# Optimization experiments

Measured on AMD Instinct MI355X. Metric: run time of the kernel, lower is better.

Reference implementation:

```python
import jax, jax.numpy as jnp
import numpy as np

N, E, D = 100000, 640000, 128  # nodes, edges, feature dim (in_dim == out_dim == 128)
BN_EPS = 1e-5


def setup_inputs() -> dict:
    key = jax.random.key(0)
    ks = jax.random.split(key, 8)
    x = jax.random.normal(ks[0], (N, D), dtype=jnp.float32)
    edge_index = jax.random.randint(ks[1], (2, E), 0, N, dtype=jnp.int64)
    s = 1.0 / np.sqrt(D)
    W1 = jax.random.uniform(ks[2], (D, D), jnp.float32, -s, s)
    b1 = jax.random.uniform(ks[3], (D,), jnp.float32, -s, s)
    W2 = jax.random.uniform(ks[4], (D, D), jnp.float32, -s, s)
    b2 = jax.random.uniform(ks[5], (D,), jnp.float32, -s, s)
    return {
        "x": x,
        "edge_index": edge_index,
        "eps": jnp.array([0.1], dtype=jnp.float32),
        "W1": W1, "b1": b1,
        "g1": jnp.ones((D,), jnp.float32), "beta1": jnp.zeros((D,), jnp.float32),
        "W2": W2, "b2": b2,
        "g2": jnp.ones((D,), jnp.float32), "beta2": jnp.zeros((D,), jnp.float32),
    }


def _batchnorm(h, gamma, beta):
    # BatchNorm1d in training mode: biased batch stats over the node dim
    mean = jnp.mean(h, axis=0)
    var = jnp.var(h, axis=0)
    return gamma * (h - mean) * jax.lax.rsqrt(var + BN_EPS) + beta


def reference(x, edge_index, eps, W1, b1, g1, beta1, W2, b2, g2, beta2):
    src, dst = edge_index[0], edge_index[1]
    # gather messages from source nodes, scatter-add into destination nodes
    aggr = jax.ops.segment_sum(x[src], dst, num_segments=x.shape[0])  # [N, D]
    h = (1.0 + eps) * x + aggr
    h = jax.nn.relu(_batchnorm(h @ W1.T + b1, g1, beta1))
    h = jax.nn.relu(_batchnorm(h @ W2.T + b2, g2, beta2))
    return h
```

## Files before the change

### kernel.cpp

```cpp
#include <hip/hip_runtime.h>

#define NN 100000
#define DD 128
#define EE 640000
#define NPAD 100352
#define NCHUNK 391

typedef __bf16 bf16x8 __attribute__((ext_vector_type(8)));
typedef float floatx4 __attribute__((ext_vector_type(4)));

union FragU { int4 i; bf16x8 b; unsigned short us[8]; };

__device__ __forceinline__ unsigned short f2bf(float f) {
    unsigned int u = __float_as_uint(f);
    u += 0x7FFF + ((u >> 16) & 1);
    return (unsigned short)(u >> 16);
}

#define HBLK 2500
#define XBLK 3200
__global__ __launch_bounds__(256) void pre_k(
    const int* __restrict__ ei, int* __restrict__ deg,
    const float4* __restrict__ x4, ushort4* __restrict__ xb4,
    const float4* __restrict__ W1, const float4* __restrict__ W2,
    ushort4* __restrict__ wb1, ushort4* __restrict__ wb2) {
    int bid = blockIdx.x;
    if (bid < HBLK) {
        int e = bid * 256 + threadIdx.x;
        atomicAdd(&deg[ei[EE + e]], 1);
    } else if (bid < HBLK + XBLK) {
        for (int i = (bid - HBLK) * 256 + threadIdx.x; i < NN * 32;
             i += XBLK * 256) {
            float4 v = x4[i];
            ushort4 u;
            u.x = f2bf(v.x); u.y = f2bf(v.y); u.z = f2bf(v.z); u.w = f2bf(v.w);
            xb4[i] = u;
        }
    } else {
        int wb = bid - HBLK - XBLK;
        const float4* src = (wb < 16) ? W1 : W2;
        ushort4* dst = (wb < 16) ? wb1 : wb2;
        int i = (wb & 15) * 256 + threadIdx.x;
        float4 v = src[i];
        ushort4 u;
        u.x = f2bf(v.x); u.y = f2bf(v.y); u.z = f2bf(v.z); u.w = f2bf(v.w);
        dst[i] = u;
    }
}

__global__ __launch_bounds__(256) void scan1_k(const int* __restrict__ deg,
                                               int* __restrict__ cursor,
                                               int* __restrict__ chunkSums) {
    __shared__ int s[256];
    int t = threadIdx.x, g = blockIdx.x * 256 + t;
    int v = (g < NN) ? deg[g] : 0;
    s[t] = v;
    __syncthreads();
    for (int off = 1; off < 256; off <<= 1) {
        int u = (t >= off) ? s[t - off] : 0;
        __syncthreads();
        s[t] += u;
        __syncthreads();
    }
    if (g < NN) cursor[g] = s[t] - v;
    if (t == 255) chunkSums[blockIdx.x] = s[255];
}

__global__ __launch_bounds__(512) void scan2_k(int* __restrict__ chunkSums,
                                               int n, float* __restrict__ stats) {
    __shared__ int s[512];
    int t = threadIdx.x;
    stats[t] = 0.f;
    int v = (t < n) ? chunkSums[t] : 0;
    s[t] = v;
    __syncthreads();
    for (int off = 1; off < 512; off <<= 1) {
        int u = (t >= off) ? s[t - off] : 0;
        __syncthreads();
        s[t] += u;
        __syncthreads();
    }
    if (t < n) chunkSums[t] = s[t] - v;
}

__global__ __launch_bounds__(256) void scan3_k(int* __restrict__ cursor,
                                               const int* __restrict__ chunkSums) {
    int g = blockIdx.x * 256 + threadIdx.x;
    if (g < NN) cursor[g] += chunkSums[blockIdx.x];
}

__global__ __launch_bounds__(256) void esort_k(const int* __restrict__ ei,
                                               int* __restrict__ cursor,
                                               int* __restrict__ ssrc) {
    int e = blockIdx.x * 256 + threadIdx.x;
    if (e >= EE) return;
    int pos = atomicAdd(&cursor[ei[EE + e]], 1);
    ssrc[pos] = ei[e];
}

__global__ __launch_bounds__(256) void aggregate_k(
    const float* __restrict__ x, const unsigned short* __restrict__ xb,
    const int* __restrict__ ssrc, const int* __restrict__ cursor,
    const int* __restrict__ deg, const float* __restrict__ epsp,
    unsigned short* __restrict__ hout) {
    int tid = blockIdx.x * 256 + threadIdx.x;
    int node = tid >> 4, lane = tid & 15;
    if (node >= NN) return;
    int d = deg[node];
    int start = cursor[node] - d;
    float ef = 1.0f + epsp[0];

    const float4* xs = (const float4*)(x + node * 128 + lane * 8);
    float4 s0 = xs[0], s1 = xs[1];
    float acc[8] = {ef * s0.x, ef * s0.y, ef * s0.z, ef * s0.w,
                    ef * s1.x, ef * s1.y, ef * s1.z, ef * s1.w};

    for (int j = 0; j < d; ++j) {
        int s = ssrc[start + j];
        int4 raw = *(const int4*)(xb + s * 128 + lane * 8);
        unsigned int u0 = (unsigned int)raw.x, u1 = (unsigned int)raw.y;
        unsigned int u2 = (unsigned int)raw.z, u3 = (unsigned int)raw.w;
        acc[0] += __uint_as_float(u0 << 16);
        acc[1] += __uint_as_float(u0 & 0xffff0000u);
        acc[2] += __uint_as_float(u1 << 16);
        acc[3] += __uint_as_float(u1 & 0xffff0000u);
        acc[4] += __uint_as_float(u2 << 16);
        acc[5] += __uint_as_float(u2 & 0xffff0000u);
        acc[6] += __uint_as_float(u3 << 16);
        acc[7] += __uint_as_float(u3 & 0xffff0000u);
    }
    FragU o;
#pragma unroll
    for (int i = 0; i < 8; ++i) o.us[i] = f2bf(acc[i]);
    *(int4*)(hout + node * 128 + lane * 8) = o.i;
}

template <int MODE>
__global__ __launch_bounds__(256) void gemm_k(
    const unsigned short* __restrict__ hA,
    float* y,
    const unsigned short* __restrict__ Wb, const float* __restrict__ bias,
    const float* __restrict__ stats_in, const float* __restrict__ g,
    const float* __restrict__ be, float* __restrict__ stats_out) {
    __shared__ float sc[128], sh[128];
    __shared__ float s_sum[128], s_sq[128];
    const int tid = threadIdx.x;
    if (tid < 128) { s_sum[tid] = 0.f; s_sq[tid] = 0.f; }
    if (MODE == 1 && tid < 128) {
        const float inv = 1.0f / (float)NN;
        float mean = stats_in[tid] * inv;
        float var = stats_in[128 + tid] * inv - mean * mean;
        float s = g[tid] * rsqrtf(var + 1e-5f);
        sc[tid] = s;
        sh[tid] = be[tid] - mean * s;
    }
    __syncthreads();

    const int rowBase = blockIdx.x * 128;
    const int l = tid & 63, w = tid >> 6;
    const int m = l & 15, q = l >> 4;

    floatx4 acc[2][8];
#pragma unroll
    for (int rt = 0; rt < 2; ++rt)
#pragma unroll
        for (int ct = 0; ct < 8; ++ct) acc[rt][ct] = (floatx4)0.0f;

#pragma unroll 1
    for (int kc = 0; kc < 4; ++kc) {
        const int k0 = kc * 32 + q * 8;
        bf16x8 a[2];
#pragma unroll
        for (int rt = 0; rt < 2; ++rt) {
            int rg = rowBase + w * 32 + rt * 16 + m;
            FragU u;
            if (MODE == 0) {
                u.i = (rg < NN) ? *(const int4*)(hA + rg * 128 + k0)
                                : make_int4(0, 0, 0, 0);
            } else {
                if (rg < NN) {
                    const float4* p = (const float4*)(y + rg * 128 + k0);
                    float4 v0 = p[0], v1 = p[1];
                    u.us[0] = f2bf(fmaxf(v0.x * sc[k0+0] + sh[k0+0], 0.f));
                    u.us[1] = f2bf(fmaxf(v0.y * sc[k0+1] + sh[k0+1], 0.f));
                    u.us[2] = f2bf(fmaxf(v0.z * sc[k0+2] + sh[k0+2], 0.f));
                    u.us[3] = f2bf(fmaxf(v0.w * sc[k0+3] + sh[k0+3], 0.f));
                    u.us[4] = f2bf(fmaxf(v1.x * sc[k0+4] + sh[k0+4], 0.f));
                    u.us[5] = f2bf(fmaxf(v1.y * sc[k0+5] + sh[k0+5], 0.f));
                    u.us[6] = f2bf(fmaxf(v1.z * sc[k0+6] + sh[k0+6], 0.f));
                    u.us[7] = f2bf(fmaxf(v1.w * sc[k0+7] + sh[k0+7], 0.f));
                } else {
                    u.i = make_int4(0, 0, 0, 0);
                }
            }
            a[rt] = u.b;
        }
#pragma unroll
        for (int ct = 0; ct < 8; ++ct) {
            bf16x8 b = *(const bf16x8*)(Wb + (ct * 16 + m) * 128 + k0);
            acc[0][ct] = __builtin_amdgcn_mfma_f32_16x16x32_bf16(a[0], b, acc[0][ct], 0, 0, 0);
            acc[1][ct] = __builtin_amdgcn_mfma_f32_16x16x32_bf16(a[1], b, acc[1][ct], 0, 0, 0);
        }
    }

#pragma unroll
    for (int ct = 0; ct < 8; ++ct) {
        int col = ct * 16 + m;
        float bc = bias[col];
        float ps = 0.f, pq = 0.f;
#pragma unroll
        for (int rt = 0; rt < 2; ++rt) {
#pragma unroll
            for (int i = 0; i < 4; ++i) {
                int rg = rowBase + w * 32 + rt * 16 + q * 4 + i;
                if (rg < NN) {
                    float yv = acc[rt][ct][i] + bc;
                    y[rg * 128 + col] = yv;
                    ps += yv;
                    pq += yv * yv;
                }
            }
        }
        atomicAdd(&s_sum[col], ps);
        atomicAdd(&s_sq[col], pq);
    }
    __syncthreads();
    if (tid < 128) {
        unsafeAtomicAdd(&stats_out[tid], s_sum[tid]);
        unsafeAtomicAdd(&stats_out[128 + tid], s_sq[tid]);
    }
}

__global__ __launch_bounds__(256) void bn_final_k(
    float* y, const float* __restrict__ stats,
    const float* __restrict__ g, const float* __restrict__ beta) {
    __shared__ __align__(16) float sc[128];
    __shared__ __align__(16) float sh[128];
    int t = threadIdx.x;
    if (t < 128) {
        const float inv = 1.0f / (float)NN;
        float mean = stats[t] * inv;
        float var = stats[128 + t] * inv - mean * mean;
        float s = g[t] * rsqrtf(var + 1e-5f);
        sc[t] = s;
        sh[t] = beta[t] - mean * s;
    }
    __syncthreads();
    const int total4 = NN * 32;
    float4* y4 = (float4*)y;
    for (int i = blockIdx.x * 256 + t; i < total4; i += gridDim.x * 256) {
        int c4 = i & 31;
        float4 v = y4[i];
        float4 s = ((const float4*)sc)[c4];
        float4 b = ((const float4*)sh)[c4];
        v.x = fmaxf(v.x * s.x + b.x, 0.f);
        v.y = fmaxf(v.y * s.y + b.y, 0.f);
        v.z = fmaxf(v.z * s.z + b.z, 0.f);
        v.w = fmaxf(v.w * s.w + b.w, 0.f);
        y4[i] = v;
    }
}

extern "C" void kernel_launch(void* const* d_in, const int* in_sizes, int n_in,
                              void* d_out, int out_size, void* d_ws, size_t ws_size,
                              hipStream_t stream) {
    const float* x   = (const float*)d_in[0];
    const int* ei    = (const int*)d_in[1];
    const float* eps = (const float*)d_in[2];
    const float* W1  = (const float*)d_in[3];
    const float* b1  = (const float*)d_in[4];
    const float* g1  = (const float*)d_in[5];
    const float* be1 = (const float*)d_in[6];
    const float* W2  = (const float*)d_in[7];
    const float* b2  = (const float*)d_in[8];
    const float* g2  = (const float*)d_in[9];
    const float* be2 = (const float*)d_in[10];
    float* out = (float*)d_out;

    int* deg        = (int*)d_ws;
    int* cursor     = deg + NPAD;
    int* chunkSums  = cursor + NPAD;
    int* ssrc       = chunkSums + 512;
    unsigned short* hbuf = (unsigned short*)(ssrc + EE);
    unsigned short* wb1  = hbuf + (size_t)NN * DD;
    unsigned short* wb2  = wb1 + 16384;
    float* stats    = (float*)(wb2 + 16384);
    unsigned short* xb = (unsigned short*)d_out;

    hipMemsetAsync(deg, 0, NPAD * sizeof(int), stream);

    pre_k<<<HBLK + XBLK + 32, 256, 0, stream>>>(
        ei, deg, (const float4*)x, (ushort4*)xb,
        (const float4*)W1, (const float4*)W2, (ushort4*)wb1, (ushort4*)wb2);
    scan1_k<<<NCHUNK, 256, 0, stream>>>(deg, cursor, chunkSums);
    scan2_k<<<1, 512, 0, stream>>>(chunkSums, NCHUNK, stats);
    scan3_k<<<NCHUNK, 256, 0, stream>>>(cursor, chunkSums);
    esort_k<<<(EE + 255) / 256, 256, 0, stream>>>(ei, cursor, ssrc);
    aggregate_k<<<(NN * 16 + 255) / 256, 256, 0, stream>>>(
        x, xb, ssrc, cursor, deg, eps, hbuf);

    const int gblocks = (NN + 127) / 128;
    gemm_k<0><<<gblocks, 256, 0, stream>>>(hbuf, out, wb1, b1,
                                           nullptr, nullptr, nullptr, stats);
    gemm_k<1><<<gblocks, 256, 0, stream>>>(nullptr, out, wb2, b2,
                                           stats, g1, be1, stats + 256);
    bn_final_k<<<4096, 256, 0, stream>>>(out, stats + 256, g2, be2);
}
```

Baseline: 366.0 us.

## Store intermediates in bf16, stage W in LDS, single-block scan, unroll gather

Replaces the three-kernel prefix scan with one 1024-thread block scan. The aggregation now reads the self term from bf16 x and unrolls the neighbor gather by four. The GEMMs stage the weight matrix in LDS, use 64-row tiles, and keep the intermediate activations in bf16 in place instead of fp32, which roughly halves intermediate traffic. Final BN reads bf16 and writes fp32. This cuts memory traffic and launch count, at the cost of extra bf16 rounding on the self term and on pre-BN activations, and a serial single-block scan.

```diff
diff --git a/kernel.cpp b/kernel.cpp
--- a/kernel.cpp
+++ b/kernel.cpp
@@ -4,7 +4,7 @@
 #define DD 128
 #define EE 640000
 #define NPAD 100352
-#define NCHUNK 391
+#define GEMM_BLOCKS 1563
 
 typedef __bf16 bf16x8 __attribute__((ext_vector_type(8)));
 typedef float floatx4 __attribute__((ext_vector_type(4)));
@@ -15,6 +15,21 @@
     unsigned int u = __float_as_uint(f);
     u += 0x7FFF + ((u >> 16) & 1);
     return (unsigned short)(u >> 16);
+}
+__device__ __forceinline__ float bf2f(unsigned short u) {
+    return __uint_as_float(((unsigned int)u) << 16);
+}
+__device__ __forceinline__ void addbf8(float* acc, int4 raw) {
+    unsigned int u0 = (unsigned int)raw.x, u1 = (unsigned int)raw.y;
+    unsigned int u2 = (unsigned int)raw.z, u3 = (unsigned int)raw.w;
+    acc[0] += __uint_as_float(u0 << 16);
+    acc[1] += __uint_as_float(u0 & 0xffff0000u);
+    acc[2] += __uint_as_float(u1 << 16);
+    acc[3] += __uint_as_float(u1 & 0xffff0000u);
+    acc[4] += __uint_as_float(u2 << 16);
+    acc[5] += __uint_as_float(u2 & 0xffff0000u);
+    acc[6] += __uint_as_float(u3 << 16);
+    acc[7] += __uint_as_float(u3 & 0xffff0000u);
 }
 
 #define HBLK 2500
@@ -48,45 +63,29 @@
     }
 }
 
-__global__ __launch_bounds__(256) void scan1_k(const int* __restrict__ deg,
-                                               int* __restrict__ cursor,
-                                               int* __restrict__ chunkSums) {
-    __shared__ int s[256];
-    int t = threadIdx.x, g = blockIdx.x * 256 + t;
-    int v = (g < NN) ? deg[g] : 0;
-    s[t] = v;
+__global__ __launch_bounds__(1024) void scan_k(
+    const int* __restrict__ deg, int* __restrict__ cursor,
+    float* __restrict__ stats) {
+    __shared__ int part[1024];
+    int t = threadIdx.x;
+    if (t < 512) stats[t] = 0.f;
+    int base = t * 98;
+    int s = 0;
+    for (int j = 0; j < 98; ++j) s += deg[base + j];
+    part[t] = s;
     __syncthreads();
-    for (int off = 1; off < 256; off <<= 1) {
-        int u = (t >= off) ? s[t - off] : 0;
+    for (int off = 1; off < 1024; off <<= 1) {
+        int u = (t >= off) ? part[t - off] : 0;
         __syncthreads();
-        s[t] += u;
+        part[t] += u;
         __syncthreads();
     }
-    if (g < NN) cursor[g] = s[t] - v;
-    if (t == 255) chunkSums[blockIdx.x] = s[255];
-}
-
-__global__ __launch_bounds__(512) void scan2_k(int* __restrict__ chunkSums,
-                                               int n, float* __restrict__ stats) {
-    __shared__ int s[512];
-    int t = threadIdx.x;
-    stats[t] = 0.f;
-    int v = (t < n) ? chunkSums[t] : 0;
-    s[t] = v;
-    __syncthreads();
-    for (int off = 1; off < 512; off <<= 1) {
-        int u = (t >= off) ? s[t - off] : 0;
-        __syncthreads();
-        s[t] += u;
-        __syncthreads();
-    }
-    if (t < n) chunkSums[t] = s[t] - v;
-}
-
-__global__ __launch_bounds__(256) void scan3_k(int* __restrict__ cursor,
-                                               const int* __restrict__ chunkSums) {
-    int g = blockIdx.x * 256 + threadIdx.x;
-    if (g < NN) cursor[g] += chunkSums[blockIdx.x];
+    int run = part[t] - s;
+    for (int j = 0; j < 98; ++j) {
+        int idx = base + j;
+        cursor[idx] = run;
+        run += deg[idx];
+    }
 }
 
 __global__ __launch_bounds__(256) void esort_k(const int* __restrict__ ei,
@@ -99,10 +98,9 @@
 }
 
 __global__ __launch_bounds__(256) void aggregate_k(
-    const float* __restrict__ x, const unsigned short* __restrict__ xb,
-    const int* __restrict__ ssrc, const int* __restrict__ cursor,
-    const int* __restrict__ deg, const float* __restrict__ epsp,
-    unsigned short* __restrict__ hout) {
+    const unsigned short* __restrict__ xb, const int* __restrict__ ssrc,
+    const int* __restrict__ cursor, const int* __restrict__ deg,
+    const float* __restrict__ epsp, unsigned short* __restrict__ hout) {
     int tid = blockIdx.x * 256 + threadIdx.x;
     int node = tid >> 4, lane = tid & 15;
     if (node >= NN) return;
@@ -110,24 +108,29 @@
     int start = cursor[node] - d;
     float ef = 1.0f + epsp[0];
 
-    const float4* xs = (const float4*)(x + node * 128 + lane * 8);
-    float4 s0 = xs[0], s1 = xs[1];
-    float acc[8] = {ef * s0.x, ef * s0.y, ef * s0.z, ef * s0.w,
-                    ef * s1.x, ef * s1.y, ef * s1.z, ef * s1.w};
-
-    for (int j = 0; j < d; ++j) {
+    float acc[8] = {0, 0, 0, 0, 0, 0, 0, 0};
+    {
+        int4 raw = *(const int4*)(xb + node * 128 + lane * 8);
+        addbf8(acc, raw);
+#pragma unroll
+        for (int i = 0; i < 8; ++i) acc[i] *= ef;
+    }
+    int j = 0;
+    for (; j + 4 <= d; j += 4) {
+        int s0 = ssrc[start + j + 0];
+        int s1 = ssrc[start + j + 1];
+        int s2 = ssrc[start + j + 2];
+        int s3 = ssrc[start + j + 3];
+        int4 r0 = *(const int4*)(xb + s0 * 128 + lane * 8);
+        int4 r1 = *(const int4*)(xb + s1 * 128 + lane * 8);
+        int4 r2 = *(const int4*)(xb + s2 * 128 + lane * 8);
+        int4 r3 = *(const int4*)(xb + s3 * 128 + lane * 8);
+        addbf8(acc, r0); addbf8(acc, r1); addbf8(acc, r2); addbf8(acc, r3);
+    }
+    for (; j < d; ++j) {
         int s = ssrc[start + j];
-        int4 raw = *(const int4*)(xb + s * 128 + lane * 8);
-        unsigned int u0 = (unsigned int)raw.x, u1 = (unsigned int)raw.y;
-        unsigned int u2 = (unsigned int)raw.z, u3 = (unsigned int)raw.w;
-        acc[0] += __uint_as_float(u0 << 16);
-        acc[1] += __uint_as_float(u0 & 0xffff0000u);
-        acc[2] += __uint_as_float(u1 << 16);
-        acc[3] += __uint_as_float(u1 & 0xffff0000u);
-        acc[4] += __uint_as_float(u2 << 16);
-        acc[5] += __uint_as_float(u2 & 0xffff0000u);
-        acc[6] += __uint_as_float(u3 << 16);
-        acc[7] += __uint_as_float(u3 & 0xffff0000u);
+        int4 r = *(const int4*)(xb + s * 128 + lane * 8);
+        addbf8(acc, r);
     }
     FragU o;
 #pragma unroll
@@ -137,69 +140,75 @@
 
 template <int MODE>
 __global__ __launch_bounds__(256) void gemm_k(
-    const unsigned short* __restrict__ hA,
-    float* y,
-    const unsigned short* __restrict__ Wb, const float* __restrict__ bias,
-    const float* __restrict__ stats_in, const float* __restrict__ g,
-    const float* __restrict__ be, float* __restrict__ stats_out) {
-    __shared__ float sc[128], sh[128];
-    __shared__ float s_sum[128], s_sq[128];
+    unsigned short* hio, const unsigned short* __restrict__ Wb,
+    const float* __restrict__ bias, const float* __restrict__ stats_in,
+    const float* __restrict__ g, const float* __restrict__ be,
+    float* __restrict__ stats_out) {
+    __shared__ __align__(16) unsigned short Bs[128][132];
+    __shared__ __align__(16) float sc[128], sh[128];
+    __shared__ __align__(16) float s_sum[128], s_sq[128];
+
     const int tid = threadIdx.x;
-    if (tid < 128) { s_sum[tid] = 0.f; s_sq[tid] = 0.f; }
-    if (MODE == 1 && tid < 128) {
-        const float inv = 1.0f / (float)NN;
-        float mean = stats_in[tid] * inv;
-        float var = stats_in[128 + tid] * inv - mean * mean;
-        float s = g[tid] * rsqrtf(var + 1e-5f);
-        sc[tid] = s;
-        sh[tid] = be[tid] - mean * s;
-    }
+    if (tid < 128) {
+        s_sum[tid] = 0.f; s_sq[tid] = 0.f;
+        if (MODE == 1) {
+            const float inv = 1.0f / (float)NN;
+            float mean = stats_in[tid] * inv;
+            float var = stats_in[128 + tid] * inv - mean * mean;
+            float s = g[tid] * rsqrtf(var + 1e-5f);
+            sc[tid] = s;
+            sh[tid] = be[tid] - mean * s;
+        }
+    }
+#pragma unroll
+    for (int it = 0; it < 8; ++it) {
+        int idx = it * 256 + tid;
+        int row = idx >> 4, c8 = (idx & 15) * 8;
+        int4 v = *(const int4*)(Wb + row * 128 + c8);
+        *(int4*)&Bs[row][c8] = v;
+    }
+
+    const int w = tid >> 6, l = tid & 63, m = l & 15, q = l >> 4;
+    const int rA = blockIdx.x * 64 + w * 16 + m;
+    const int rAc = (rA < NN) ? rA : (NN - 1);
+
+    FragU a[4];
+#pragma unroll
+    for (int kc = 0; kc < 4; ++kc)
+        a[kc].i = *(const int4*)(hio + rAc * 128 + kc * 32 + q * 8);
+
     __syncthreads();
 
-    const int rowBase = blockIdx.x * 128;
-    const int l = tid & 63, w = tid >> 6;
-    const int m = l & 15, q = l >> 4;
-
-    floatx4 acc[2][8];
-#pragma unroll
-    for (int rt = 0; rt < 2; ++rt)
-#pragma unroll
-        for (int ct = 0; ct < 8; ++ct) acc[rt][ct] = (floatx4)0.0f;
-
-#pragma unroll 1
+    if (MODE == 1) {
+#pragma unroll
+        for (int kc = 0; kc < 4; ++kc) {
+            int k0 = kc * 32 + q * 8;
+            float4 sA = *(const float4*)&sc[k0], sB = *(const float4*)&sc[k0 + 4];
+            float4 hA = *(const float4*)&sh[k0], hB = *(const float4*)&sh[k0 + 4];
+            FragU u = a[kc];
+            u.us[0] = f2bf(fmaxf(bf2f(u.us[0]) * sA.x + hA.x, 0.f));
+            u.us[1] = f2bf(fmaxf(bf2f(u.us[1]) * sA.y + hA.y, 0.f));
+            u.us[2] = f2bf(fmaxf(bf2f(u.us[2]) * sA.z + hA.z, 0.f));
+            u.us[3] = f2bf(fmaxf(bf2f(u.us[3]) * sA.w + hA.w, 0.f));
+            u.us[4] = f2bf(fmaxf(bf2f(u.us[4]) * sB.x + hB.x, 0.f));
+            u.us[5] = f2bf(fmaxf(bf2f(u.us[5]) * sB.y + hB.y, 0.f));
+            u.us[6] = f2bf(fmaxf(bf2f(u.us[6]) * sB.z + hB.z, 0.f));
+            u.us[7] = f2bf(fmaxf(bf2f(u.us[7]) * sB.w + hB.w, 0.f));
+            a[kc] = u;
+        }
+    }
+
+    floatx4 acc[8];
+#pragma unroll
+    for (int ct = 0; ct < 8; ++ct) acc[ct] = (floatx4)0.0f;
+
+#pragma unroll
     for (int kc = 0; kc < 4; ++kc) {
-        const int k0 = kc * 32 + q * 8;
-        bf16x8 a[2];
-#pragma unroll
-        for (int rt = 0; rt < 2; ++rt) {
-            int rg = rowBase + w * 32 + rt * 16 + m;
-            FragU u;
-            if (MODE == 0) {
-                u.i = (rg < NN) ? *(const int4*)(hA + rg * 128 + k0)
-                                : make_int4(0, 0, 0, 0);
-            } else {
-                if (rg < NN) {
-                    const float4* p = (const float4*)(y + rg * 128 + k0);
-                    float4 v0 = p[0], v1 = p[1];
-                    u.us[0] = f2bf(fmaxf(v0.x * sc[k0+0] + sh[k0+0], 0.f));
-                    u.us[1] = f2bf(fmaxf(v0.y * sc[k0+1] + sh[k0+1], 0.f));
-                    u.us[2] = f2bf(fmaxf(v0.z * sc[k0+2] + sh[k0+2], 0.f));
-                    u.us[3] = f2bf(fmaxf(v0.w * sc[k0+3] + sh[k0+3], 0.f));
-                    u.us[4] = f2bf(fmaxf(v1.x * sc[k0+4] + sh[k0+4], 0.f));
-                    u.us[5] = f2bf(fmaxf(v1.y * sc[k0+5] + sh[k0+5], 0.f));
-                    u.us[6] = f2bf(fmaxf(v1.z * sc[k0+6] + sh[k0+6], 0.f));
-                    u.us[7] = f2bf(fmaxf(v1.w * sc[k0+7] + sh[k0+7], 0.f));
-                } else {
-                    u.i = make_int4(0, 0, 0, 0);
-                }
-            }
-            a[rt] = u.b;
-        }
+        int k0 = kc * 32 + q * 8;
 #pragma unroll
         for (int ct = 0; ct < 8; ++ct) {
-            bf16x8 b = *(const bf16x8*)(Wb + (ct * 16 + m) * 128 + k0);
-            acc[0][ct] = __builtin_amdgcn_mfma_f32_16x16x32_bf16(a[0], b, acc[0][ct], 0, 0, 0);
-            acc[1][ct] = __builtin_amdgcn_mfma_f32_16x16x32_bf16(a[1], b, acc[1][ct], 0, 0, 0);
+            bf16x8 b = *(const bf16x8*)&Bs[ct * 16 + m][k0];
+            acc[ct] = __builtin_amdgcn_mfma_f32_16x16x32_bf16(a[kc].b, b, acc[ct], 0, 0, 0);
         }
     }
 
@@ -209,16 +218,13 @@
         float bc = bias[col];
         float ps = 0.f, pq = 0.f;
 #pragma unroll
-        for (int rt = 0; rt < 2; ++rt) {
-#pragma unroll
-            for (int i = 0; i < 4; ++i) {
-                int rg = rowBase + w * 32 + rt * 16 + q * 4 + i;
-                if (rg < NN) {
-                    float yv = acc[rt][ct][i] + bc;
-                    y[rg * 128 + col] = yv;
-                    ps += yv;
-                    pq += yv * yv;
-                }
+        for (int i = 0; i < 4; ++i) {
+            int rg = blockIdx.x * 64 + w * 16 + q * 4 + i;
+            if (rg < NN) {
+                float yv = acc[ct][i] + bc;
+                hio[rg * 128 + col] = f2bf(yv);
+                ps += yv;
+                pq += yv * yv;
             }
         }
         atomicAdd(&s_sum[col], ps);
@@ -232,8 +238,9 @@
 }
 
 __global__ __launch_bounds__(256) void bn_final_k(
-    float* y, const float* __restrict__ stats,
-    const float* __restrict__ g, const float* __restrict__ beta) {
+    const unsigned short* __restrict__ y, float* __restrict__ out,
+    const float* __restrict__ stats, const float* __restrict__ g,
+    const float* __restrict__ beta) {
     __shared__ __align__(16) float sc[128];
     __shared__ __align__(16) float sh[128];
     int t = threadIdx.x;
@@ -246,19 +253,24 @@
         sh[t] = beta[t] - mean * s;
     }
     __syncthreads();
-    const int total4 = NN * 32;
-    float4* y4 = (float4*)y;
-    for (int i = blockIdx.x * 256 + t; i < total4; i += gridDim.x * 256) {
-        int c4 = i & 31;
-        float4 v = y4[i];
-        float4 s = ((const float4*)sc)[c4];
-        float4 b = ((const float4*)sh)[c4];
-        v.x = fmaxf(v.x * s.x + b.x, 0.f);
-        v.y = fmaxf(v.y * s.y + b.y, 0.f);
-        v.z = fmaxf(v.z * s.z + b.z, 0.f);
-        v.w = fmaxf(v.w * s.w + b.w, 0.f);
-        y4[i] = v;
-    }
+    int i = blockIdx.x * 256 + t;
+    int c8 = (i & 15) * 8;
+    int4 raw = ((const int4*)y)[i];
+    float v[8] = {0, 0, 0, 0, 0, 0, 0, 0};
+    addbf8(v, raw);
+    float4 sA = *(const float4*)&sc[c8], sB = *(const float4*)&sc[c8 + 4];
+    float4 hA = *(const float4*)&sh[c8], hB = *(const float4*)&sh[c8 + 4];
+    float4 o0, o1;
+    o0.x = fmaxf(v[0] * sA.x + hA.x, 0.f);
+    o0.y = fmaxf(v[1] * sA.y + hA.y, 0.f);
+    o0.z = fmaxf(v[2] * sA.z + hA.z, 0.f);
+    o0.w = fmaxf(v[3] * sA.w + hA.w, 0.f);
+    o1.x = fmaxf(v[4] * sB.x + hB.x, 0.f);
+    o1.y = fmaxf(v[5] * sB.y + hB.y, 0.f);
+    o1.z = fmaxf(v[6] * sB.z + hB.z, 0.f);
+    o1.w = fmaxf(v[7] * sB.w + hB.w, 0.f);
+    ((float4*)out)[i * 2] = o0;
+    ((float4*)out)[i * 2 + 1] = o1;
 }
 
 extern "C" void kernel_launch(void* const* d_in, const int* in_sizes, int n_in,
@@ -277,14 +289,13 @@
     const float* be2 = (const float*)d_in[10];
     float* out = (float*)d_out;
 
-    int* deg        = (int*)d_ws;
-    int* cursor     = deg + NPAD;
-    int* chunkSums  = cursor + NPAD;
-    int* ssrc       = chunkSums + 512;
+    int* deg    = (int*)d_ws;
+    int* cursor = deg + NPAD;
+    int* ssrc   = cursor + NPAD;
     unsigned short* hbuf = (unsigned short*)(ssrc + EE);
     unsigned short* wb1  = hbuf + (size_t)NN * DD;
     unsigned short* wb2  = wb1 + 16384;
-    float* stats    = (float*)(wb2 + 16384);
+    float* stats = (float*)(wb2 + 16384);
     unsigned short* xb = (unsigned short*)d_out;
 
     hipMemsetAsync(deg, 0, NPAD * sizeof(int), stream);
@@ -292,17 +303,14 @@
     pre_k<<<HBLK + XBLK + 32, 256, 0, stream>>>(
         ei, deg, (const float4*)x, (ushort4*)xb,
         (const float4*)W1, (const float4*)W2, (ushort4*)wb1, (ushort4*)wb2);
-    scan1_k<<<NCHUNK, 256, 0, stream>>>(deg, cursor, chunkSums);
-    scan2_k<<<1, 512, 0, stream>>>(chunkSums, NCHUNK, stats);
-    scan3_k<<<NCHUNK, 256, 0, stream>>>(cursor, chunkSums);
+    scan_k<<<1, 1024, 0, stream>>>(deg, cursor, stats);
     esort_k<<<(EE + 255) / 256, 256, 0, stream>>>(ei, cursor, ssrc);
-    aggregate_k<<<(NN * 16 + 255) / 256, 256, 0, stream>>>(
-        x, xb, ssrc, cursor, deg, eps, hbuf);
-
-    const int gblocks = (NN + 127) / 128;
-    gemm_k<0><<<gblocks, 256, 0, stream>>>(hbuf, out, wb1, b1,
-                                           nullptr, nullptr, nullptr, stats);
-    gemm_k<1><<<gblocks, 256, 0, stream>>>(nullptr, out, wb2, b2,
-                                           stats, g1, be1, stats + 256);
-    bn_final_k<<<4096, 256, 0, stream>>>(out, stats + 256, g2, be2);
-}
+    aggregate_k<<<NN * 16 / 256, 256, 0, stream>>>(xb, ssrc, cursor, deg, eps,
+                                                   hbuf);
+    gemm_k<0><<<GEMM_BLOCKS, 256, 0, stream>>>(hbuf, wb1, b1, nullptr, nullptr,
+                                               nullptr, stats);
+    gemm_k<1><<<GEMM_BLOCKS, 256, 0, stream>>>(hbuf, wb2, b2, stats, g1, be1,
+                                               stats + 256);
+    bn_final_k<<<NN * 16 / 256, 256, 0, stream>>>(hbuf, out, stats + 256, g2,
+                                                  be2);
+}
```

New measurement: 377.4 us. +3.1%, slower.
